# Performance work log

Measured on AMD Instinct MI355X. Metric: run time of the kernel, lower is better.

The kernel has to match this reference:

```python
import jax, jax.numpy as jnp
import numpy as np
from jax.ops import segment_sum, segment_max

N = 50000
E = 800000
IN_C, HID_C, OUT_C, HEADS = 64, 128, 32, 4
BN_EPS = 1e-5
NEG_SLOPE = 0.2


def setup_inputs() -> dict:
    key = jax.random.key(0)
    ks = jax.random.split(key, 16)
    s = 0.1  # weight scale for numerical sanity
    inp = {
        'x': jax.random.normal(ks[0], (N, IN_C), jnp.float32),
        'edge_index': jax.random.randint(ks[1], (2, E), 0, N, jnp.int64),
        'sage1_wl': jax.random.normal(ks[2], (IN_C, HID_C), jnp.float32) * s,
        'sage1_bl': jnp.zeros((HID_C,), jnp.float32),
        'sage1_wr': jax.random.normal(ks[3], (IN_C, HID_C), jnp.float32) * s,
        'bn1_gamma': jnp.ones((HID_C,), jnp.float32),
        'bn1_beta': jnp.zeros((HID_C,), jnp.float32),
        'bn1_mean': jnp.zeros((HID_C,), jnp.float32),
        'bn1_var': jnp.ones((HID_C,), jnp.float32),
        'sage2_wl': jax.random.normal(ks[4], (HID_C, HID_C), jnp.float32) * s,
        'sage2_bl': jnp.zeros((HID_C,), jnp.float32),
        'sage2_wr': jax.random.normal(ks[5], (HID_C, HID_C), jnp.float32) * s,
        'bn2_gamma': jnp.ones((HID_C,), jnp.float32),
        'bn2_beta': jnp.zeros((HID_C,), jnp.float32),
        'bn2_mean': jnp.zeros((HID_C,), jnp.float32),
        'bn2_var': jnp.ones((HID_C,), jnp.float32),
        'gat_w': jax.random.normal(ks[6], (HID_C, HEADS * OUT_C), jnp.float32) * s,
        'gat_att_src': jax.random.normal(ks[7], (HEADS, OUT_C), jnp.float32) * s,
        'gat_att_dst': jax.random.normal(ks[8], (HEADS, OUT_C), jnp.float32) * s,
        'gat_bias': jnp.zeros((OUT_C,), jnp.float32),
        'cls_w1': jax.random.normal(ks[9], (OUT_C, 64), jnp.float32) * s,
        'cls_b1': jnp.zeros((64,), jnp.float32),
        'cls_w2': jax.random.normal(ks[10], (64, 1), jnp.float32) * s,
        'cls_b2': jnp.zeros((1,), jnp.float32),
    }
    return inp


def _sage_conv(x, src, dst, n, wl, bl, wr):
    # PyG SAGEConv (mean aggr): lin_l(mean_{j in N(i)} x_j) + lin_r(x_i)
    agg = segment_sum(x[src], dst, num_segments=n)           # [N, C]
    cnt = segment_sum(jnp.ones((src.shape[0], 1), x.dtype), dst, num_segments=n)
    mean = agg / jnp.maximum(cnt, 1.0)
    return mean @ wl + bl + x @ wr


def _bn_eval(x, gamma, beta, mean, var):
    return (x - mean) * jax.lax.rsqrt(var + BN_EPS) * gamma + beta


def _gat_conv(x, src, dst, n, w, att_src, att_dst, bias):
    # PyG GATConv, concat=False (head-average), add_self_loops=True
    loop = jnp.arange(n, dtype=src.dtype)
    s = jnp.concatenate([src, loop])
    d = jnp.concatenate([dst, loop])
    h = (x @ w).reshape(n, HEADS, OUT_C)                     # [N, H, C]
    a_src = jnp.einsum('nhc,hc->nh', h, att_src)             # [N, H]
    a_dst = jnp.einsum('nhc,hc->nh', h, att_dst)             # [N, H]
    e = jax.nn.leaky_relu(a_src[s] + a_dst[d], NEG_SLOPE)    # [Etot, H]
    m = segment_max(e, d, num_segments=n)                    # stable softmax per dst
    ex = jnp.exp(e - m[d])
    den = segment_sum(ex, d, num_segments=n)
    alpha = ex / den[d]                                      # [Etot, H]
    out = segment_sum(alpha[:, :, None] * h[s], d, num_segments=n)  # [N, H, C]
    return out.mean(axis=1) + bias                           # concat=False -> mean over heads


def reference(x, edge_index,
              sage1_wl, sage1_bl, sage1_wr,
              bn1_gamma, bn1_beta, bn1_mean, bn1_var,
              sage2_wl, sage2_bl, sage2_wr,
              bn2_gamma, bn2_beta, bn2_mean, bn2_var,
              gat_w, gat_att_src, gat_att_dst, gat_bias,
              cls_w1, cls_b1, cls_w2, cls_b2):
    n = x.shape[0]
    src, dst = edge_index[0], edge_index[1]
    # Layer 0: SAGE(64->128) + BN + ReLU (no residual: shapes differ); dropout = eval noop
    h = _sage_conv(x, src, dst, n, sage1_wl, sage1_bl, sage1_wr)
    h = jax.nn.relu(_bn_eval(h, bn1_gamma, bn1_beta, bn1_mean, bn1_var))
    # Layer 1: SAGE(128->128) + BN + residual + ReLU
    identity = h
    h2 = _sage_conv(h, src, dst, n, sage2_wl, sage2_bl, sage2_wr)
    h2 = _bn_eval(h2, bn2_gamma, bn2_beta, bn2_mean, bn2_var) + identity
    h2 = jax.nn.relu(h2)
    # Final layer: GAT head (128 -> 32, 4 heads averaged)
    embeddings = _gat_conv(h2, src, dst, n, gat_w, gat_att_src, gat_att_dst, gat_bias)
    # MLP classifier (dropout eval noop)
    logits = jax.nn.relu(embeddings @ cls_w1 + cls_b1) @ cls_w2 + cls_b2
    return embeddings, logits
```

## Files before the change

kernel.cpp:

```cpp
#include <hip/hip_runtime.h>

typedef unsigned int uint_t;
typedef unsigned short ush;
typedef short bf16x8 __attribute__((ext_vector_type(8)));
typedef float f32x4 __attribute__((ext_vector_type(4)));

constexpr int TPB = 256;
#define LOG2E 1.4426950408889634f

__device__ __forceinline__ float lrelu(float x){ return fmaxf(x, 0.f) + 0.2f*fminf(x, 0.f); }
__device__ __forceinline__ ush f2b(float f){
  uint_t u = __float_as_uint(f);
  return (ush)((u + 0x7fffu + ((u >> 16) & 1u)) >> 16);
}
__device__ __forceinline__ float b2f(ush s){ return __uint_as_float(((uint_t)s) << 16); }
__device__ __forceinline__ float blo(uint_t u){ return __uint_as_float(u << 16); }
__device__ __forceinline__ float bhi(uint_t u){ return __uint_as_float(u & 0xffff0000u); }

__global__ void k_bnfold(const float* __restrict__ g1, const float* __restrict__ b1,
                         const float* __restrict__ m1, const float* __restrict__ v1,
                         const float* __restrict__ g2, const float* __restrict__ b2,
                         const float* __restrict__ m2, const float* __restrict__ v2,
                         float* __restrict__ out){
  int t = threadIdx.x;
  int o = t & 127;
  bool second = t >= 128;
  const float* g = second ? g2 : g1;  const float* b = second ? b2 : b1;
  const float* m = second ? m2 : m1;  const float* v = second ? v2 : v1;
  float sc = g[o] * rsqrtf(v[o] + 1e-5f);
  float sh = b[o] - m[o]*sc;
  int off = second ? 256 : 0;
  out[off + o] = sc;
  out[off + 128 + o] = sh;
}

__global__ void k_deg(const int* __restrict__ dst, int* __restrict__ degi, int E){
  int t = blockIdx.x*TPB + threadIdx.x;
  if (t < E) atomicAdd(&degi[dst[t]], 1);
}

__global__ __launch_bounds__(1024) void k_scan1(const int* __restrict__ deg,
                                                int* __restrict__ out,
                                                int* __restrict__ bsum, int n){
  __shared__ int ws[16];
  int tid = threadIdx.x;
  int gid = blockIdx.x*1024 + tid;
  int v = (gid < n) ? deg[gid] : 0;
  int lane = tid & 63, wid = tid >> 6;
  int s = v;
  for (int off = 1; off < 64; off <<= 1){
    int t2 = __shfl_up(s, off);
    if (lane >= off) s += t2;
  }
  if (lane == 63) ws[wid] = s;
  __syncthreads();
  if (wid == 0){
    int w = (lane < 16) ? ws[lane] : 0;
    for (int off = 1; off < 16; off <<= 1){
      int t2 = __shfl_up(w, off);
      if (lane >= off) w += t2;
    }
    if (lane < 16) ws[lane] = w;
  }
  __syncthreads();
  int base = wid > 0 ? ws[wid-1] : 0;
  int incl = base + s;
  if (gid < n) out[gid] = incl - v;
  if (tid == 1023) bsum[blockIdx.x] = incl;
}

__global__ void k_scan2(int* __restrict__ bsum, int nb){
  int lane = threadIdx.x;
  int carry = 0;
  for (int base = 0; base < nb; base += 64){
    int i = base + lane;
    int v = (i < nb) ? bsum[i] : 0;
    int s = v;
    for (int off = 1; off < 64; off <<= 1){
      int t2 = __shfl_up(s, off);
      if (lane >= off) s += t2;
    }
    if (i < nb) bsum[i] = carry + s - v;
    int tot = __shfl(s, 63);
    carry += tot;
  }
  if (lane == 0) bsum[nb] = carry;
}

__global__ void k_scan3(int* __restrict__ offs, const int* __restrict__ bsum, int n, int nb){
  int gid = blockIdx.x*TPB + threadIdx.x;
  if (gid < n) offs[gid] += bsum[gid >> 10];
  else if (gid == n) offs[n] = bsum[nb];
}

__global__ void k_fill(const int* __restrict__ src, const int* __restrict__ dst,
                       const int* __restrict__ offs, int* __restrict__ cur,
                       int* __restrict__ esrc, int E){
  int t = blockIdx.x*TPB + threadIdx.x;
  if (t >= E) return;
  int d = dst[t];
  int p = offs[d] + atomicAdd(&cur[d], 1);
  esrc[p] = src[t];
}

__global__ void k_tobf16(const float* __restrict__ in, ush* __restrict__ out, int n4){
  int t = blockIdx.x*TPB + threadIdx.x;
  if (t >= n4) return;
  float4 v = *(const float4*)(in + (size_t)t*4);
  ushort4 o;
  o.x = f2b(v.x); o.y = f2b(v.y); o.z = f2b(v.z); o.w = f2b(v.w);
  *(ushort4*)(out + (size_t)t*4) = o;
}

__global__ void k_wprep(const float* __restrict__ wr, const float* __restrict__ wl,
                        int C1, int K, ush* __restrict__ WT){
  int t = blockIdx.x*TPB + threadIdx.x;
  if (t >= 128*K) return;
  int n = t / K, k = t % K;
  float v = (k < C1) ? wr[(size_t)k*128 + n] : wl[(size_t)(k - C1)*128 + n];
  WT[t] = f2b(v);
}

template<int C>
__global__ __launch_bounds__(256) void k_gather_mean_b(
    const int* __restrict__ offs, const int* __restrict__ esrc,
    const uint_t* __restrict__ xb, uint_t* __restrict__ meanb, int n){
  constexpr int L = C/2;
  int tid = threadIdx.x;
  int nid = blockIdx.x*(256/L) + tid/L;
  int l = tid % L;
  if (nid >= n) return;
  int k0 = offs[nid], k1 = offs[nid+1];
  const int* sp = esrc + k0;
  int cnt = k1 - k0;
  float s0 = 0.f, s1 = 0.f;
  int k = 0;
  for (; k + 8 <= cnt; k += 8){
    int e0 = sp[k],   e1 = sp[k+1], e2 = sp[k+2], e3 = sp[k+3];
    int e4 = sp[k+4], e5 = sp[k+5], e6 = sp[k+6], e7 = sp[k+7];
    uint_t u0 = xb[(size_t)e0*L + l];
    uint_t u1 = xb[(size_t)e1*L + l];
    uint_t u2 = xb[(size_t)e2*L + l];
    uint_t u3 = xb[(size_t)e3*L + l];
    uint_t u4 = xb[(size_t)e4*L + l];
    uint_t u5 = xb[(size_t)e5*L + l];
    uint_t u6 = xb[(size_t)e6*L + l];
    uint_t u7 = xb[(size_t)e7*L + l];
    s0 += ((blo(u0) + blo(u1)) + (blo(u2) + blo(u3)))
        + ((blo(u4) + blo(u5)) + (blo(u6) + blo(u7)));
    s1 += ((bhi(u0) + bhi(u1)) + (bhi(u2) + bhi(u3)))
        + ((bhi(u4) + bhi(u5)) + (bhi(u6) + bhi(u7)));
  }
  for (; k + 4 <= cnt; k += 4){
    int e0 = sp[k], e1 = sp[k+1], e2 = sp[k+2], e3 = sp[k+3];
    uint_t u0 = xb[(size_t)e0*L + l];
    uint_t u1 = xb[(size_t)e1*L + l];
    uint_t u2 = xb[(size_t)e2*L + l];
    uint_t u3 = xb[(size_t)e3*L + l];
    s0 += (blo(u0) + blo(u1)) + (blo(u2) + blo(u3));
    s1 += (bhi(u0) + bhi(u1)) + (bhi(u2) + bhi(u3));
  }
  for (; k < cnt; ++k){
    uint_t u = xb[(size_t)sp[k]*L + l];
    s0 += blo(u);
    s1 += bhi(u);
  }
  float inv = 1.f / (float)max(cnt, 1);
  uint_t lo = f2b(s0*inv), hi = f2b(s1*inv);
  meanb[(size_t)nid*L + l] = lo | (hi << 16);
}

template<int K, bool BN, bool RES, bool RELU>
__global__ __launch_bounds__(256) void k_mm_mfma(
    const ush* __restrict__ A1, int C1,
    const ush* __restrict__ A2,
    const ush* __restrict__ WT,
    const float* __restrict__ bias,
    const float* __restrict__ bnp, int bnoff,
    const float* __restrict__ res,
    float* __restrict__ out, ush* __restrict__ outb, int n)
{
  constexpr int PAD = K + 8;
  __shared__ ush sA[32][PAD];
  int tid = threadIdx.x;
  int wave = tid >> 6, lane = tid & 63;
  int node0 = blockIdx.x * 32;
  int C2 = K - C1;

  for (int idx = tid; idx < 32*(K/8); idx += 256) {
    int r  = idx / (K/8);
    int kc = (idx % (K/8)) * 8;
    int g = node0 + r;
    uint4 v = make_uint4(0,0,0,0);
    if (g < n) {
      if (kc < C1) v = *(const uint4*)(A1 + (size_t)g*C1 + kc);
      else         v = *(const uint4*)(A2 + (size_t)g*C2 + (kc - C1));
    }
    *(uint4*)&sA[r][kc] = v;
  }
  __syncthreads();

  f32x4 acc[2][2] = {};
  int l15 = lane & 15, lk = (lane >> 4) * 8;
  const ush* wt0 = WT + (size_t)(wave*32 + l15) * K + lk;
  const ush* wt1 = wt0 + (size_t)16 * K;

  #pragma unroll
  for (int kk = 0; kk < K; kk += 32) {
    bf16x8 a0 = *(const bf16x8*)&sA[l15][kk + lk];
    bf16x8 a1 = *(const bf16x8*)&sA[16 + l15][kk + lk];
    bf16x8 b0 = *(const bf16x8*)(wt0 + kk);
    bf16x8 b1 = *(const bf16x8*)(wt1 + kk);
    acc[0][0] = __builtin_amdgcn_mfma_f32_16x16x32_bf16(a0, b0, acc[0][0], 0, 0, 0);
    acc[0][1] = __builtin_amdgcn_mfma_f32_16x16x32_bf16(a0, b1, acc[0][1], 0, 0, 0);
    acc[1][0] = __builtin_amdgcn_mfma_f32_16x16x32_bf16(a1, b0, acc[1][0], 0, 0, 0);
    acc[1][1] = __builtin_amdgcn_mfma_f32_16x16x32_bf16(a1, b1, acc[1][1], 0, 0, 0);
  }

  int r0 = (lane >> 4) * 4;
  #pragma unroll
  for (int mt = 0; mt < 2; ++mt) {
    #pragma unroll
    for (int nt = 0; nt < 2; ++nt) {
      int nn = wave*32 + nt*16 + l15;
      float bv = bias ? bias[nn] : 0.f;
      float sc = 1.f, sh = 0.f;
      if constexpr (BN) { sc = bnp[bnoff + nn]; sh = bnp[bnoff + 128 + nn]; }
      #pragma unroll
      for (int j = 0; j < 4; ++j) {
        int g = node0 + mt*16 + r0 + j;
        if (g < n) {
          float v = acc[mt][nt][j] + bv;
          if constexpr (BN)   v = v*sc + sh;
          if constexpr (RES)  v += res[(size_t)g*128 + nn];
          if constexpr (RELU) v = fmaxf(v, 0.f);
          if (out)  out[(size_t)g*128 + nn] = v;
          if (outb) outb[(size_t)g*128 + nn] = f2b(v);
        }
      }
    }
  }
}

__global__ void k_attn(const uint_t* __restrict__ hgb, const float* __restrict__ atts,
                       const float* __restrict__ attd, float* __restrict__ asrc,
                       float* __restrict__ adst, int n){
  int t = blockIdx.x*TPB + threadIdx.x;
  if (t >= n*4) return;
  int nid = t >> 2, h = t & 3;
  const uint_t* hp = hgb + (size_t)nid*64 + h*16;
  float as = 0.f, ad = 0.f;
  #pragma unroll
  for (int i = 0; i < 16; ++i) {
    uint_t u = hp[i];
    float v0 = blo(u);
    float v1 = bhi(u);
    as = fmaf(v0, atts[h*32 + 2*i],     as);
    as = fmaf(v1, atts[h*32 + 2*i + 1], as);
    ad = fmaf(v0, attd[h*32 + 2*i],     ad);
    ad = fmaf(v1, attd[h*32 + 2*i + 1], ad);
  }
  asrc[t] = as * LOG2E; adst[t] = ad * LOG2E;
}

__global__ __launch_bounds__(256) void k_gat(
    const int* __restrict__ offs, const int* __restrict__ esrc,
    const float* __restrict__ asrc, const float* __restrict__ adst,
    const uint_t* __restrict__ hgb, const float* __restrict__ gbias,
    const float* __restrict__ w1, const float* __restrict__ b1,
    const float* __restrict__ w2, const float* __restrict__ b2,
    float* __restrict__ out_emb, float* __restrict__ out_log, int n){
  __shared__ float semb[4][32];
  int tid = threadIdx.x;
  int wl = tid >> 6;
  int l = tid & 63;
  int nid = blockIdx.x*4 + wl;
  if (nid >= n) return;
  int h = l >> 4;
  int j16 = l & 15;
  int hb = l & 48;
  int i4 = nid*4 + h;
  float ad = adst[i4];
  float e0 = exp2f(lrelu(asrc[i4] + ad));
  uint_t u = hgb[(size_t)nid*64 + l];
  float accD  = e0;
  float accN0 = e0 * blo(u);
  float accN1 = e0 * bhi(u);
  int k0 = offs[nid], k1 = offs[nid+1];
  const int* sp = esrc + k0;
  int cnt = k1 - k0;
  int k = 0;
  for (; k + 16 <= cnt; k += 16){
    int mys = sp[k + j16];
    float mye = exp2f(lrelu(asrc[mys*4 + h] + ad));
    #pragma unroll
    for (int j = 0; j < 16; ++j){
      float e = __shfl(mye, hb | j);
      int s   = sp[k + j];
      uint_t v = hgb[(size_t)s*64 + l];
      accD += e;
      accN0 = fmaf(e, blo(v), accN0);
      accN1 = fmaf(e, bhi(v), accN1);
    }
  }
  if (k + 8 <= cnt){
    int mys = sp[k + (j16 & 7)];
    float mye = exp2f(lrelu(asrc[mys*4 + h] + ad));
    #pragma unroll
    for (int j = 0; j < 8; ++j){
      float e = __shfl(mye, hb | j);
      int s   = sp[k + j];
      uint_t v = hgb[(size_t)s*64 + l];
      accD += e;
      accN0 = fmaf(e, blo(v), accN0);
      accN1 = fmaf(e, bhi(v), accN1);
    }
    k += 8;
  }
  for (; k < cnt; ++k){
    int s = sp[k];
    float e = exp2f(lrelu(asrc[s*4 + h] + ad));
    uint_t v = hgb[(size_t)s*64 + l];
    accD += e;
    accN0 = fmaf(e, blo(v), accN0);
    accN1 = fmaf(e, bhi(v), accN1);
  }
  float inv = 1.f / accD;
  float v0 = accN0 * inv, v1 = accN1 * inv;
  v0 += __shfl_xor(v0, 16); v0 += __shfl_xor(v0, 32);
  v1 += __shfl_xor(v1, 16); v1 += __shfl_xor(v1, 32);
  if (l < 16){
    int c = l*2;
    float2 o;
    o.x = 0.25f*v0 + gbias[c];
    o.y = 0.25f*v1 + gbias[c+1];
    *(float2*)(out_emb + (size_t)nid*32 + c) = o;
    semb[wl][c] = o.x;
    semb[wl][c+1] = o.y;
  }
  float a = b1[l];
  #pragma unroll
  for (int c = 0; c < 32; ++c) a = fmaf(semb[wl][c], w1[c*64 + l], a);
  float t = fmaxf(a, 0.f) * w2[l];
  t += __shfl_xor(t, 1);  t += __shfl_xor(t, 2);  t += __shfl_xor(t, 4);
  t += __shfl_xor(t, 8);  t += __shfl_xor(t, 16); t += __shfl_xor(t, 32);
  if (l == 0) out_log[nid] = t + b2[0];
}

extern "C" void kernel_launch(void* const* d_in, const int* in_sizes, int n_in,
                              void* d_out, int out_size, void* d_ws, size_t ws_size,
                              hipStream_t stream) {
  const float* x    = (const float*)d_in[0];
  const int*   ei   = (const int*)  d_in[1];
  const float* s1wl = (const float*)d_in[2];
  const float* s1bl = (const float*)d_in[3];
  const float* s1wr = (const float*)d_in[4];
  const float* bn1g = (const float*)d_in[5];
  const float* bn1b = (const float*)d_in[6];
  const float* bn1m = (const float*)d_in[7];
  const float* bn1v = (const float*)d_in[8];
  const float* s2wl = (const float*)d_in[9];
  const float* s2bl = (const float*)d_in[10];
  const float* s2wr = (const float*)d_in[11];
  const float* bn2g = (const float*)d_in[12];
  const float* bn2b = (const float*)d_in[13];
  const float* bn2m = (const float*)d_in[14];
  const float* bn2v = (const float*)d_in[15];
  const float* gatw = (const float*)d_in[16];
  const float* atts = (const float*)d_in[17];
  const float* attd = (const float*)d_in[18];
  const float* gatb = (const float*)d_in[19];
  const float* cw1  = (const float*)d_in[20];
  const float* cb1  = (const float*)d_in[21];
  const float* cw2  = (const float*)d_in[22];
  const float* cb2  = (const float*)d_in[23];

  const int N = in_sizes[0] / 64;
  const int E = in_sizes[1] / 2;
  const int* src = ei;
  const int* dst = ei + E;
  const int NBK = (N + 1023) / 1024;

  float* h1   = (float*)d_ws;
  float* asrc = h1 + (size_t)N*128;
  float* adst = asrc + (size_t)N*4;
  float* bnp  = adst + (size_t)N*4;
  ush* regA = (ush*)(bnp + 512);
  ush* regB = regA + (size_t)N*128;
  ush* regC = regB + (size_t)N*128;
  ush* W1T  = regC + (size_t)N*128;
  ush* W2T  = W1T + 128*128;
  ush* WGT  = W2T + 128*256;
  int* degi = (int*)(WGT + 128*128);
  int* offs = degi + N;
  int* cur  = offs + N + 1;
  int* esrc = cur + N;
  int* bsum = esrc + E;

  ush* xb     = regA;
  ush* mean1b = regA + (size_t)N*64;
  ush* mean2b = regA;
  ush* h1b    = regB;
  ush* hgb    = regB;
  ush* h2b    = regC;

  float* out_emb = (float*)d_out;
  float* out_log = out_emb + (size_t)N*32;

  hipMemsetAsync(degi, 0, (size_t)N*4, stream);
  hipMemsetAsync(cur,  0, (size_t)N*4, stream);

  k_bnfold<<<1, 256, 0, stream>>>(bn1g,bn1b,bn1m,bn1v, bn2g,bn2b,bn2m,bn2v, bnp);

  k_deg<<<(E+TPB-1)/TPB, TPB, 0, stream>>>(dst, degi, E);
  k_scan1<<<NBK, 1024, 0, stream>>>(degi, offs, bsum, N);
  k_scan2<<<1, 64, 0, stream>>>(bsum, NBK);
  k_scan3<<<(N+1+TPB-1)/TPB, TPB, 0, stream>>>(offs, bsum, N, NBK);
  k_fill<<<(E+TPB-1)/TPB, TPB, 0, stream>>>(src, dst, offs, cur, esrc, E);

  k_wprep<<<(128*128+TPB-1)/TPB, TPB, 0, stream>>>(s1wr, s1wl, 64, 128, W1T);
  k_wprep<<<(128*256+TPB-1)/TPB, TPB, 0, stream>>>(s2wr, s2wl, 128, 256, W2T);
  k_wprep<<<(128*128+TPB-1)/TPB, TPB, 0, stream>>>(gatw, nullptr, 128, 128, WGT);

  k_tobf16<<<(N*16+TPB-1)/TPB, TPB, 0, stream>>>(x, xb, N*16);

  int nmm = (N + 31) / 32;

  k_gather_mean_b<64><<<(N+7)/8, 256, 0, stream>>>(offs, esrc, (const uint_t*)xb, (uint_t*)mean1b, N);
  k_mm_mfma<128,true,false,true><<<nmm, 256, 0, stream>>>(
      xb, 64, mean1b, W1T, s1bl, bnp, 0, nullptr, h1, h1b, N);

  k_gather_mean_b<128><<<(N+3)/4, 256, 0, stream>>>(offs, esrc, (const uint_t*)h1b, (uint_t*)mean2b, N);
  k_mm_mfma<256,true,true,true><<<nmm, 256, 0, stream>>>(
      h1b, 128, mean2b, W2T, s2bl, bnp, 256, h1, nullptr, h2b, N);

  k_mm_mfma<128,false,false,false><<<nmm, 256, 0, stream>>>(
      h2b, 128, nullptr, WGT, nullptr, bnp, 0, nullptr, nullptr, hgb, N);

  k_attn<<<(N*4+TPB-1)/TPB, TPB, 0, stream>>>((const uint_t*)hgb, atts, attd, asrc, adst, N);
  k_gat<<<(N+3)/4, 256, 0, stream>>>(offs, esrc, asrc, adst, (const uint_t*)hgb, gatb,
                                     cw1, cb1, cw2, cb2, out_emb, out_log, N);
}
```

Baseline: 294.1 us.

## Read residual from staged bf16 LDS tile and simplify GAT edge loop

The first SAGE matmul no longer writes an fp32 copy of h1. The second matmul takes its residual from the bf16 h1 columns already staged in shared memory, which removes a 25.6 MB fp32 write and read. The GAT aggregation loop swaps its shuffle-based 16/8-edge batching for a plain 4-way unrolled loop, where each lane computes the exponentials directly. The residual now uses bf16-rounded values (slight precision loss), and the GAT loop recomputes each exp per lane instead of sharing it across the wave.

```diff
diff --git a/kernel.cpp b/kernel.cpp
--- a/kernel.cpp
+++ b/kernel.cpp
@@ -170,15 +170,14 @@
   meanb[(size_t)nid*L + l] = lo | (hi << 16);
 }
 
-template<int K, bool BN, bool RES, bool RELU>
+template<int K, bool BN, bool RES_LDS, bool RELU>
 __global__ __launch_bounds__(256) void k_mm_mfma(
     const ush* __restrict__ A1, int C1,
     const ush* __restrict__ A2,
     const ush* __restrict__ WT,
     const float* __restrict__ bias,
     const float* __restrict__ bnp, int bnoff,
-    const float* __restrict__ res,
-    float* __restrict__ out, ush* __restrict__ outb, int n)
+    ush* __restrict__ outb, int n)
 {
   constexpr int PAD = K + 8;
   __shared__ ush sA[32][PAD];
@@ -228,14 +227,14 @@
       if constexpr (BN) { sc = bnp[bnoff + nn]; sh = bnp[bnoff + 128 + nn]; }
       #pragma unroll
       for (int j = 0; j < 4; ++j) {
-        int g = node0 + mt*16 + r0 + j;
+        int r = mt*16 + r0 + j;
+        int g = node0 + r;
         if (g < n) {
           float v = acc[mt][nt][j] + bv;
-          if constexpr (BN)   v = v*sc + sh;
-          if constexpr (RES)  v += res[(size_t)g*128 + nn];
-          if constexpr (RELU) v = fmaxf(v, 0.f);
-          if (out)  out[(size_t)g*128 + nn] = v;
-          if (outb) outb[(size_t)g*128 + nn] = f2b(v);
+          if constexpr (BN)      v = v*sc + sh;
+          if constexpr (RES_LDS) v += b2f(sA[r][nn]);
+          if constexpr (RELU)    v = fmaxf(v, 0.f);
+          outb[(size_t)g*128 + nn] = f2b(v);
         }
       }
     }
@@ -277,8 +276,6 @@
   int nid = blockIdx.x*4 + wl;
   if (nid >= n) return;
   int h = l >> 4;
-  int j16 = l & 15;
-  int hb = l & 48;
   int i4 = nid*4 + h;
   float ad = adst[i4];
   float e0 = exp2f(lrelu(asrc[i4] + ad));
@@ -290,32 +287,27 @@
   const int* sp = esrc + k0;
   int cnt = k1 - k0;
   int k = 0;
-  for (; k + 16 <= cnt; k += 16){
-    int mys = sp[k + j16];
-    float mye = exp2f(lrelu(asrc[mys*4 + h] + ad));
-    #pragma unroll
-    for (int j = 0; j < 16; ++j){
-      float e = __shfl(mye, hb | j);
-      int s   = sp[k + j];
-      uint_t v = hgb[(size_t)s*64 + l];
-      accD += e;
-      accN0 = fmaf(e, blo(v), accN0);
-      accN1 = fmaf(e, bhi(v), accN1);
-    }
-  }
-  if (k + 8 <= cnt){
-    int mys = sp[k + (j16 & 7)];
-    float mye = exp2f(lrelu(asrc[mys*4 + h] + ad));
-    #pragma unroll
-    for (int j = 0; j < 8; ++j){
-      float e = __shfl(mye, hb | j);
-      int s   = sp[k + j];
-      uint_t v = hgb[(size_t)s*64 + l];
-      accD += e;
-      accN0 = fmaf(e, blo(v), accN0);
-      accN1 = fmaf(e, bhi(v), accN1);
-    }
-    k += 8;
+  for (; k + 4 <= cnt; k += 4){
+    int s0 = sp[k], s1 = sp[k+1], s2 = sp[k+2], s3 = sp[k+3];
+    float a0 = asrc[s0*4 + h], a1 = asrc[s1*4 + h];
+    float a2 = asrc[s2*4 + h], a3 = asrc[s3*4 + h];
+    uint_t v0 = hgb[(size_t)s0*64 + l];
+    uint_t v1 = hgb[(size_t)s1*64 + l];
+    uint_t v2 = hgb[(size_t)s2*64 + l];
+    uint_t v3 = hgb[(size_t)s3*64 + l];
+    float e0_ = exp2f(lrelu(a0 + ad));
+    float e1_ = exp2f(lrelu(a1 + ad));
+    float e2_ = exp2f(lrelu(a2 + ad));
+    float e3_ = exp2f(lrelu(a3 + ad));
+    accD += (e0_ + e1_) + (e2_ + e3_);
+    accN0 = fmaf(e0_, blo(v0), accN0);
+    accN0 = fmaf(e1_, blo(v1), accN0);
+    accN0 = fmaf(e2_, blo(v2), accN0);
+    accN0 = fmaf(e3_, blo(v3), accN0);
+    accN1 = fmaf(e0_, bhi(v0), accN1);
+    accN1 = fmaf(e1_, bhi(v1), accN1);
+    accN1 = fmaf(e2_, bhi(v2), accN1);
+    accN1 = fmaf(e3_, bhi(v3), accN1);
   }
   for (; k < cnt; ++k){
     int s = sp[k];
@@ -381,8 +373,7 @@
   const int* dst = ei + E;
   const int NBK = (N + 1023) / 1024;
 
-  float* h1   = (float*)d_ws;
-  float* asrc = h1 + (size_t)N*128;
+  float* asrc = (float*)d_ws;
   float* adst = asrc + (size_t)N*4;
   float* bnp  = adst + (size_t)N*4;
   ush* regA = (ush*)(bnp + 512);
@@ -428,14 +419,14 @@
 
   k_gather_mean_b<64><<<(N+7)/8, 256, 0, stream>>>(offs, esrc, (const uint_t*)xb, (uint_t*)mean1b, N);
   k_mm_mfma<128,true,false,true><<<nmm, 256, 0, stream>>>(
-      xb, 64, mean1b, W1T, s1bl, bnp, 0, nullptr, h1, h1b, N);
+      xb, 64, mean1b, W1T, s1bl, bnp, 0, h1b, N);
 
   k_gather_mean_b<128><<<(N+3)/4, 256, 0, stream>>>(offs, esrc, (const uint_t*)h1b, (uint_t*)mean2b, N);
   k_mm_mfma<256,true,true,true><<<nmm, 256, 0, stream>>>(
-      h1b, 128, mean2b, W2T, s2bl, bnp, 256, h1, nullptr, h2b, N);
+      h1b, 128, mean2b, W2T, s2bl, bnp, 256, h2b, N);
 
   k_mm_mfma<128,false,false,false><<<nmm, 256, 0, stream>>>(
-      h2b, 128, nullptr, WGT, nullptr, bnp, 0, nullptr, nullptr, hgb, N);
+      h2b, 128, nullptr, WGT, nullptr, bnp, 0, hgb, N);
 
   k_attn<<<(N*4+TPB-1)/TPB, TPB, 0, stream>>>((const uint_t*)hgb, atts, attd, asrc, adst, N);
   k_gat<<<(N+3)/4, 256, 0, stream>>>(offs, esrc, asrc, adst, (const uint_t*)hgb, gatb,
```

After: 272.0 us. -7.5%, faster.
